# Kernel tuning notes

Hardware: AMD Instinct MI355X
Metric: run time of the kernel (lower is better)

The kernel has to match this reference:

```python
import jax, jax.numpy as jnp
import numpy as np


def build_entangle(n):
    """Fixed entangling unitary: ring of CNOTs composed with H on every qubit.
    Real-valued 2^n x 2^n matrix (all gates real)."""
    D = 1 << n
    H = np.array([[1.0, 1.0], [1.0, -1.0]], np.float32) / np.float32(np.sqrt(2.0))
    Hn = np.array([[1.0]], np.float32)
    for _ in range(n):
        Hn = np.kron(Hn, H)
    # CNOT ring as a permutation of basis states (qubit 0 = most significant bit)
    idx = np.arange(D)
    pairs = [(i, i + 1) for i in range(n - 1)] + [(n - 1, 0)]
    for c, t in pairs:
        bit = (idx >> (n - 1 - c)) & 1
        idx = idx ^ (bit << (n - 1 - t))
    E = np.empty((D, D), np.float32)
    E[idx] = Hn  # P @ Hn where P|b> = |perm(b)>
    return jnp.asarray(E)


def setup_inputs() -> dict:
    key = jax.random.key(0)
    k1, k2 = jax.random.split(key)
    B, C, L = 8, 3, 2048
    K = 3
    n = C * K  # 9 qubits
    O = 8      # out_channels
    x = jax.random.normal(k1, (B, C, L), dtype=jnp.float32)
    theta = jax.random.normal(k2, (O, n), dtype=jnp.float32)  # one RY layer per output channel
    entangle = build_entangle(n)
    return {"x": x, "entangle": entangle, "theta": theta}


def _ry(t):
    c, s = jnp.cos(t / 2), jnp.sin(t / 2)
    return jnp.stack([jnp.stack([c, -s]), jnp.stack([s, c])])  # [2,2]


def reference(x, entangle, theta):
    B, C, L = x.shape
    O, n = theta.shape
    K = n // C
    D = 1 << n
    Lout = L - K + 1

    # im2col: unfold last dim, concat channels along last axis -> rows of length C*K
    win = jnp.arange(Lout)[:, None] + jnp.arange(K)[None, :]
    cols = x[:, :, win]                                   # [B, C, Lout, K]
    cols = cols.transpose(0, 2, 1, 3).reshape(B * Lout, n)  # [N, n]
    N = B * Lout

    # angle-encode each row as product state prod_i RY(x_i)|0> (real amplitudes)
    c = jnp.cos(cols / 2)
    s = jnp.sin(cols / 2)
    state = jnp.ones((N, 1), x.dtype)
    for i in range(n):  # fixed small loop over qubits
        amp = jnp.stack([c[:, i], s[:, i]], axis=-1)      # [N, 2]
        state = (state[:, :, None] * amp[:, None, :]).reshape(N, -1)
    # shared entangling layer (same for every output channel)
    state = state @ entangle.T                            # [N, D]

    def channel(th):
        st = state
        for i in range(n):  # learnable per-qubit RY layer
            g = _ry(th[i])
            st = st.reshape(N, 1 << i, 2, -1)
            st = jnp.einsum('ab,nlbr->nlar', g, st).reshape(N, D)
        st = st @ entangle.T
        p = st.reshape(N, 2, D // 2)
        return jnp.sum(p[:, 0] ** 2, -1) - jnp.sum(p[:, 1] ** 2, -1)  # <Z_0>, [N]

    out = jax.vmap(channel)(theta)                        # [O, N]
    return out.reshape(O, B, Lout).transpose(1, 0, 2)     # [B, O, Lout]
```

## Files before the change

kernel.cpp:

```cpp
#include <hip/hip_runtime.h>

#define Bq   8
#define Lx   2048
#define Oo   8
#define LOUT 2046
#define WPB  16
#define CPR  128

#define DPP_XOR1 0xB1
#define DPP_XOR2 0x4E
template<int CTRL>
__device__ __forceinline__ float dppf(float x) {
    int i = __float_as_int(x);
    return __int_as_float(__builtin_amdgcn_update_dpp(i, i, CTRL, 0xF, 0xF, true));
}

__global__ __launch_bounds__(512) void qconv(const float* __restrict__ x,
                                             const float* __restrict__ theta,
                                             float* __restrict__ out) {
    __shared__ float sw0[3][WPB + 2], sw1[3][WPB + 2];
    __shared__ float sC[8][9], sS[8][9];

    const int tid   = threadIdx.x;
    const int row   = blockIdx.x >> 7;
    const int chunk = blockIdx.x & (CPR - 1);
    const int l0    = chunk * WPB;

    if (tid < 3 * (WPB + 2)) {
        int c = tid / (WPB + 2), p = tid - c * (WPB + 2);
        int pos = l0 + p;
        if (pos > Lx - 1) pos = Lx - 1;
        float a = 0.5f * x[row * (3 * Lx) + c * Lx + pos];
        float sn, cs;
        __sincosf(a, &sn, &cs);
        sw0[c][p] = (cs + sn) * 0.70710678118654752f;
        sw1[c][p] = (cs - sn) * 0.70710678118654752f;
    } else if (tid >= 64 && tid < 128) {
        int idx = tid - 64;
        int o = idx >> 3, j = idx & 7;
        float th = theta[o * 9 + 8 - j];
        float sn, cs;
        __sincosf(th, &sn, &cs);
        sC[o][j] = cs;
        sS[o][j] = sn;
    }
    __syncthreads();

    const int a0  = tid & 1, b0 = (tid >> 1) & 1;
    const int o   = (tid >> 2) & 7;
    const int win = tid >> 5;
    const int l   = l0 + win;

    float w0[9], w1[9], C[8], S[8];
#pragma unroll
    for (int f = 0; f < 9; ++f) {
        const int c = f / 3, k = f - c * 3;
        w0[f] = sw0[c][win + k];
        w1[f] = sw1[c][win + k];
    }
#pragma unroll
    for (int j = 0; j < 8; ++j) { C[j] = sC[o][j]; S[j] = sS[o][j]; }

    float wa0 = a0 ? w1[8] : w0[8], wa1 = a0 ? w0[8] : w1[8];
    float wb0 = b0 ? w1[8] : w0[8], wb1 = b0 ? w0[8] : w1[8];
    float B00 = (a0 ^ b0) ? C[0] : (a0 ? -S[0] : S[0]);
    float ra0 = B00 * wa0, ra1 = B00 * wa1;
    float r00 = ra0 * wb0, r01 = ra0 * wb1, r10 = ra1 * wb0, r11 = ra1 * wb1;

#pragma unroll
    for (int j = 1; j <= 6; ++j) {
        const float u0 = w0[8 - j], u1 = w1[8 - j];
        float t00 = S[j] * r00, t01 = C[j] * r01;
        float t10 = C[j] * r10, t11 = -S[j] * r11;
        float z00 = fmaf(u0, t00, u1 * t10), z10 = fmaf(u1, t00, u0 * t10);
        float z01 = fmaf(u0, t01, u1 * t11), z11 = fmaf(u1, t01, u0 * t11);
        r00 = fmaf(u0, z00, u1 * z01); r01 = fmaf(u1, z00, u0 * z01);
        r10 = fmaf(u0, z10, u1 * z11); r11 = fmaf(u1, z10, u0 * z11);
    }

    float t00 = S[7] * r00, t01 = C[7] * r01;
    float t10 = C[7] * r10, t11 = -S[7] * r11;
    float p0 = a0 ? w1[1] : w0[1], p1 = a0 ? w0[1] : w1[1];
    float q0 = b0 ? w1[1] : w0[1], q1 = b0 ? w0[1] : w1[1];
    float A0 = (a0 ? w1[0] : w0[0]) * (b0 ? w1[0] : w0[0]);
    float A1 = (a0 ? w0[0] : w1[0]) * (b0 ? w0[0] : w1[0]);
    float term1 = fmaf(p0, fmaf(q0, t00, q1 * t01), p1 * fmaf(q0, t10, q1 * t11));
    float term2 = fmaf(p1, fmaf(q1, t00, q0 * t01), p0 * fmaf(q1, t10, q0 * t11));
    float acc = fmaf(A0, term1, A1 * term2);

    acc += dppf<DPP_XOR1>(acc);
    acc += dppf<DPP_XOR2>(acc);

    if (l < LOUT && (tid & 3) == 0)
        out[row * (Oo * LOUT) + o * LOUT + l] = acc;
}

extern "C" void kernel_launch(void* const* d_in, const int* in_sizes, int n_in,
                              void* d_out, int out_size, void* d_ws, size_t ws_size,
                              hipStream_t stream) {
    const float* x     = (const float*)d_in[0];
    const float* theta = (const float*)d_in[2];
    float* o = (float*)d_out;

    hipLaunchKernelGGL(qconv, dim3(Bq * CPR), dim3(512), 0, stream, x, theta, o);
}
```

Measured before the change: 58.65 us.

## Fold four-lane split into one thread per output using symmetric pair algebra

Each output (o, l) was previously computed by four lanes, one per (a0,b0) term, and combined with two DPP reductions. Now a single thread computes all four terms. It exploits symmetry between the (0,0)/(1,1) and (0,1)/(1,0) cases to share work through the a/d/b recurrences, which removes the cross-lane reduction and the redundant lanes. Block work grows to 64 windows per block with 32 chunks per row, and the shared-memory arrays become float2 for paired loads. In exchange each thread carries more registers and serial FLOPs, and the grid drops to 256 blocks, which may underfill the GPU.

```diff
diff --git a/kernel.cpp b/kernel.cpp
--- a/kernel.cpp
+++ b/kernel.cpp
@@ -4,25 +4,17 @@
 #define Lx   2048
 #define Oo   8
 #define LOUT 2046
-#define WPB  16
-#define CPR  128
-
-#define DPP_XOR1 0xB1
-#define DPP_XOR2 0x4E
-template<int CTRL>
-__device__ __forceinline__ float dppf(float x) {
-    int i = __float_as_int(x);
-    return __int_as_float(__builtin_amdgcn_update_dpp(i, i, CTRL, 0xF, 0xF, true));
-}
+#define WPB  64
+#define CPR  32
 
 __global__ __launch_bounds__(512) void qconv(const float* __restrict__ x,
                                              const float* __restrict__ theta,
                                              float* __restrict__ out) {
-    __shared__ float sw0[3][WPB + 2], sw1[3][WPB + 2];
-    __shared__ float sC[8][9], sS[8][9];
+    __shared__ float2 sw[3][WPB + 2];
+    __shared__ float2 st[8][8];
 
     const int tid   = threadIdx.x;
-    const int row   = blockIdx.x >> 7;
+    const int row   = blockIdx.x >> 5;
     const int chunk = blockIdx.x & (CPR - 1);
     const int l0    = chunk * WPB;
 
@@ -33,65 +25,93 @@
         float a = 0.5f * x[row * (3 * Lx) + c * Lx + pos];
         float sn, cs;
         __sincosf(a, &sn, &cs);
-        sw0[c][p] = (cs + sn) * 0.70710678118654752f;
-        sw1[c][p] = (cs - sn) * 0.70710678118654752f;
-    } else if (tid >= 64 && tid < 128) {
-        int idx = tid - 64;
+        sw[c][p] = make_float2((cs + sn) * 0.70710678118654752f,
+                               (cs - sn) * 0.70710678118654752f);
+    } else if (tid >= 256 && tid < 320) {
+        int idx = tid - 256;
         int o = idx >> 3, j = idx & 7;
         float th = theta[o * 9 + 8 - j];
         float sn, cs;
         __sincosf(th, &sn, &cs);
-        sC[o][j] = cs;
-        sS[o][j] = sn;
+        st[o][j] = make_float2(cs, sn);
     }
     __syncthreads();
 
-    const int a0  = tid & 1, b0 = (tid >> 1) & 1;
-    const int o   = (tid >> 2) & 7;
-    const int win = tid >> 5;
+    const int o   = tid & 7;
+    const int win = tid >> 3;
     const int l   = l0 + win;
 
     float w0[9], w1[9], C[8], S[8];
 #pragma unroll
     for (int f = 0; f < 9; ++f) {
         const int c = f / 3, k = f - c * 3;
-        w0[f] = sw0[c][win + k];
-        w1[f] = sw1[c][win + k];
+        float2 v = sw[c][win + k];
+        w0[f] = v.x; w1[f] = v.y;
     }
 #pragma unroll
-    for (int j = 0; j < 8; ++j) { C[j] = sC[o][j]; S[j] = sS[o][j]; }
+    for (int j = 0; j < 8; ++j) { float2 v = st[o][j]; C[j] = v.x; S[j] = v.y; }
 
-    float wa0 = a0 ? w1[8] : w0[8], wa1 = a0 ? w0[8] : w1[8];
-    float wb0 = b0 ? w1[8] : w0[8], wb1 = b0 ? w0[8] : w1[8];
-    float B00 = (a0 ^ b0) ? C[0] : (a0 ? -S[0] : S[0]);
-    float ra0 = B00 * wa0, ra1 = B00 * wa1;
-    float r00 = ra0 * wb0, r01 = ra0 * wb1, r10 = ra1 * wb0, r11 = ra1 * wb1;
+    const float e0 = w0[8], e1 = w1[8];
+    const float p00 = e0 * e0, p01 = e0 * e1, p11 = e1 * e1;
+    const float S0 = S[0], C0 = C[0];
+    float a00 = S0 * p00, a01 = S0 * p01, a11 = S0 * p11;
+    float d00 = -S0 * p11, d01 = -S0 * p01, d11 = -S0 * p00;
+    float b00 = C0 * p01, b01 = C0 * p00, b10 = C0 * p11, b11 = b00;
 
 #pragma unroll
     for (int j = 1; j <= 6; ++j) {
         const float u0 = w0[8 - j], u1 = w1[8 - j];
-        float t00 = S[j] * r00, t01 = C[j] * r01;
-        float t10 = C[j] * r10, t11 = -S[j] * r11;
-        float z00 = fmaf(u0, t00, u1 * t10), z10 = fmaf(u1, t00, u0 * t10);
-        float z01 = fmaf(u0, t01, u1 * t11), z11 = fmaf(u1, t01, u0 * t11);
-        r00 = fmaf(u0, z00, u1 * z01); r01 = fmaf(u1, z00, u0 * z01);
-        r10 = fmaf(u0, z10, u1 * z11); r11 = fmaf(u1, z10, u0 * z11);
+        const float Sj = S[j], Cj = C[j];
+        const float s0 = u0 * Sj, s1 = u1 * Sj, c0 = u0 * Cj, c1 = u1 * Cj;
+
+        float zA00 = fmaf(s0, a00, c1 * a01);
+        float zA10 = fmaf(s1, a00, c0 * a01);
+        float zA01 = fmaf(c0, a01, -(s1 * a11));
+        float zA11 = fmaf(c1, a01, -(s0 * a11));
+        a00 = fmaf(u0, zA00, u1 * zA01);
+        a01 = fmaf(u1, zA00, u0 * zA01);
+        a11 = fmaf(u1, zA10, u0 * zA11);
+
+        float zD00 = fmaf(s0, d00, c1 * d01);
+        float zD10 = fmaf(s1, d00, c0 * d01);
+        float zD01 = fmaf(c0, d01, -(s1 * d11));
+        float zD11 = fmaf(c1, d01, -(s0 * d11));
+        d00 = fmaf(u0, zD00, u1 * zD01);
+        d01 = fmaf(u1, zD00, u0 * zD01);
+        d11 = fmaf(u1, zD10, u0 * zD11);
+
+        float zB00 = fmaf(s0, b00, c1 * b10);
+        float zB10 = fmaf(s1, b00, c0 * b10);
+        float zB01 = fmaf(c0, b01, -(s1 * b11));
+        float zB11 = fmaf(c1, b01, -(s0 * b11));
+        b00 = fmaf(u0, zB00, u1 * zB01);
+        b01 = fmaf(u1, zB00, u0 * zB01);
+        b10 = fmaf(u0, zB10, u1 * zB11);
+        b11 = fmaf(u1, zB10, u0 * zB11);
     }
 
-    float t00 = S[7] * r00, t01 = C[7] * r01;
-    float t10 = C[7] * r10, t11 = -S[7] * r11;
-    float p0 = a0 ? w1[1] : w0[1], p1 = a0 ? w0[1] : w1[1];
-    float q0 = b0 ? w1[1] : w0[1], q1 = b0 ? w0[1] : w1[1];
-    float A0 = (a0 ? w1[0] : w0[0]) * (b0 ? w1[0] : w0[0]);
-    float A1 = (a0 ? w0[0] : w1[0]) * (b0 ? w0[0] : w1[0]);
-    float term1 = fmaf(p0, fmaf(q0, t00, q1 * t01), p1 * fmaf(q0, t10, q1 * t11));
-    float term2 = fmaf(p1, fmaf(q1, t00, q0 * t01), p0 * fmaf(q1, t10, q0 * t11));
-    float acc = fmaf(A0, term1, A1 * term2);
+    const float S7 = S[7], C7 = C[7];
+    const float g0 = w0[1], g1 = w1[1];
+    const float h0 = w0[0], h1 = w1[0];
+    const float hh0 = h0 * h0, hh1 = h1 * h1, hh01 = h0 * h1;
 
-    acc += dppf<DPP_XOR1>(acc);
-    acc += dppf<DPP_XOR2>(acc);
+    float tA00 = S7 * a00, tA01 = C7 * a01, tA11 = -S7 * a11;
+    float termA1 = fmaf(g0, fmaf(g0, tA00, g1 * tA01), g1 * fmaf(g0, tA01, g1 * tA11));
+    float termA2 = fmaf(g1, fmaf(g1, tA00, g0 * tA01), g0 * fmaf(g1, tA01, g0 * tA11));
+    float acc = fmaf(hh0, termA1, hh1 * termA2);
 
-    if (l < LOUT && (tid & 3) == 0)
+    float tD00 = S7 * d00, tD01 = C7 * d01, tD11 = -S7 * d11;
+    float termD1 = fmaf(g1, fmaf(g1, tD00, g0 * tD01), g0 * fmaf(g1, tD01, g0 * tD11));
+    float termD2 = fmaf(g0, fmaf(g0, tD00, g1 * tD01), g1 * fmaf(g0, tD01, g1 * tD11));
+    acc = fmaf(hh1, termD1, acc);
+    acc = fmaf(hh0, termD2, acc);
+
+    float tB00 = S7 * b00, tB01 = C7 * b01, tB10 = C7 * b10, tB11 = -S7 * b11;
+    float termB1 = fmaf(g0, fmaf(g1, tB00, g0 * tB01), g1 * fmaf(g1, tB10, g0 * tB11));
+    float termB2 = fmaf(g1, fmaf(g0, tB00, g1 * tB01), g0 * fmaf(g0, tB10, g1 * tB11));
+    acc = fmaf(2.0f * hh01, termB1 + termB2, acc);
+
+    if (l < LOUT)
         out[row * (Oo * LOUT) + o * LOUT + l] = acc;
 }
 
```

Result: faster. 57.07 us (-2.7%).
